# Performance work log

Measured on AMD Instinct MI355X. Metric: run time of the kernel, lower is better.

## Reference

```python
import jax, jax.numpy as jnp
import numpy as np

jax.config.update("jax_enable_x64", True)

# ---- physical constants (verbatim from source) ----
R = 0.000865
CONST = 2 * np.pi * R ** 3
C_SOUND = 343.0
RHO = 1.225
C1 = CONST * (1 / (6 * RHO * C_SOUND ** 2))
C2 = CONST * (-RHO / 4)
AREA = 0.0008
F = 40000.0
KWAV = 2 * np.pi / (C_SOUND / F)
W = 2 * np.pi * F
U = 3.086
M = 64
N = 64
B = 32768


def _h_of_r(rnorm):
    # h(r) = Area * (j rho c k) * u * exp(-j k r) / (2 pi r)
    return AREA * (1j * RHO * C_SOUND * KWAV) * U * np.exp(-1j * KWAV * rnorm) / (2 * np.pi * rnorm)


def _build_operators():
    # 8x8 transducer array (1cm pitch) at z=0; 8x8 focal points at z=0.10m
    xs = (np.arange(8) - 3.5) * 0.01
    gx, gy = np.meshgrid(xs, xs, indexing="ij")
    sensor_positions = np.stack([gx.ravel(), gy.ravel(), np.zeros(N)], axis=1)  # [n,3]
    fx = (np.arange(8) - 3.5) * 0.005
    px, py = np.meshgrid(fx, fx, indexing="ij")
    point_positions = np.stack([px.ravel(), py.ravel(), np.full(M, 0.10)], axis=1)  # [m,3]

    diff = point_positions[:, None, :] - sensor_positions[None, :, :]  # [m,n,3]
    r = np.linalg.norm(diff, axis=-1)
    h = _h_of_r(r)  # [m,n] complex128 (row vector h_matrices[i][0,:])

    delta = 1e-6
    q = np.empty((M, 3, N), dtype=np.complex128)
    for d in range(3):
        e = np.zeros(3)
        e[d] = delta
        rp = np.linalg.norm(diff + e, axis=-1)
        rm = np.linalg.norm(diff - e, axis=-1)
        q[:, d, :] = (-1 / (1j * W * RHO)) * (_h_of_r(rp) - _h_of_r(rm)) / (2 * delta)
    return h, q


def setup_inputs() -> dict:
    key = jax.random.key(0)
    k1, k2, k3 = jax.random.split(key, 3)
    pred_amplitude = jax.random.uniform(k1, (B, N), dtype=jnp.float32)
    pred_phase = jax.random.uniform(k2, (B, N), dtype=jnp.float32) * (2 * np.pi)
    true_energy = jax.random.normal(k3, (B, M), dtype=jnp.float32)
    h_np, q_np = _build_operators()
    return {
        "pred_amplitude": pred_amplitude,
        "pred_phase": pred_phase,
        "true_energy": true_energy,
        "h": jnp.asarray(h_np),  # [m,n] complex128
        "q": jnp.asarray(q_np),  # [m,3,n] complex128
    }


def reference(pred_amplitude, pred_phase, true_energy, h, q):
    # A_b = amplitude * exp(j*phase), cast to complex128 as in the source
    A = (pred_amplitude * jnp.exp(1j * pred_phase.astype(jnp.complex64))).astype(jnp.complex128)  # [B,n]
    # E[b,i] = Re( A^H (c1 h_i^H h_i + c2 q_i^H q_i) A )
    #        = c1 |h_i . A_b|^2 + c2 ||q_i A_b||^2   (rank-1 / rank-3 quadratic forms)
    hA = jnp.einsum("mn,bn->bm", h, A)          # [B,m]
    qA = jnp.einsum("mdn,bn->bmd", q, A)        # [B,m,3]
    E = C1 * (jnp.abs(hA) ** 2) + C2 * jnp.sum(jnp.abs(qA) ** 2, axis=-1)  # [B,m] real
    pred_energy = (E * 100000.0).astype(jnp.float32)
    return jnp.mean((pred_energy - true_energy) ** 2)
```

## Files before the change

kernel.cpp:

```cpp
#include <hip/hip_runtime.h>
#include <hip/hip_bf16.h>


typedef short s16x8 __attribute__((ext_vector_type(8)));
typedef float f32x4 __attribute__((ext_vector_type(4)));
typedef unsigned int u32x4 __attribute__((ext_vector_type(4)));

#define B_TOTAL 32768

constexpr double PI_ = 3.14159265358979323846;
constexpr double RHO_ = 1.225, CS_ = 343.0, FREQ_ = 40000.0, UU_ = 3.086, AREA_ = 0.0008;
constexpr double KW_ = 2.0 * PI_ * FREQ_ / CS_;
constexpr double WW_ = 2.0 * PI_ * FREQ_;
constexpr double RR_ = 0.000865;
constexpr double CONSTV_ = 2.0 * PI_ * RR_ * RR_ * RR_;
constexpr double C1E5_ = CONSTV_ / (6.0 * RHO_ * CS_ * CS_) * 100000.0;
constexpr double C2E5_ = CONSTV_ * RHO_ / 4.0 * 100000.0;
constexpr double GG_ = AREA_ * RHO_ * CS_ * KW_ * UU_ / (2.0 * PI_);

__device__ inline unsigned int pk2(float a, float b) {
    __hip_bfloat162 h = __float22bfloat162_rn(make_float2(a, b));
    unsigned int u;
    __builtin_memcpy(&u, &h, 4);
    return u;
}

__device__ inline void poly_sincos(float u, float& s, float& c) {
    float u2 = u * u;
    float sp = fmaf(u2, -7.6471637e-13f, 1.6059044e-10f);
    sp = fmaf(u2, sp, -2.5052108e-8f);
    sp = fmaf(u2, sp, 2.7557319e-6f);
    sp = fmaf(u2, sp, -1.9841270e-4f);
    sp = fmaf(u2, sp, 8.3333335e-3f);
    sp = fmaf(u2, sp, -0.16666667f);
    s = u * fmaf(u2, sp, 1.0f);
    float cp = fmaf(u2, -1.1470746e-11f, 2.0876757e-9f);
    cp = fmaf(u2, cp, -2.7557319e-7f);
    cp = fmaf(u2, cp, 2.4801587e-5f);
    cp = fmaf(u2, cp, -1.3888889e-3f);
    cp = fmaf(u2, cp, 4.1666668e-2f);
    cp = fmaf(u2, cp, -0.5f);
    c = fmaf(u2, cp, 1.0f);
}

__device__ inline void sincos_2pit(float t, float& s, float& c) {
    float x = t - rintf(t);
    poly_sincos(x * 6.2831853e+0f, s, c);
}

__device__ inline void sincos_rad(float p, float& s, float& c) {
    const float INV2PI = 0.15915494309189535f;
    float n = rintf(p * INV2PI);
    poly_sincos(fmaf(n, -6.2831853e+0f, p), s, c);
}

__global__ __launch_bounds__(512, 2)
void fused_energy(const float* __restrict__ amp, const float* __restrict__ ph,
                  const float* __restrict__ te,
                  double* __restrict__ partials) {
    __shared__ unsigned short Wl[512 * 128];
    __shared__ unsigned short Xt[2][32 * 128];
    __shared__ double sred[8];

    const int t = threadIdx.x;
    const int wave = t >> 6, lane = t & 63;
    const int lrow = lane & 15, lkgrp = lane >> 4;
    const int wr = wave & 3, wc = wave >> 2;
    const int blk = blockIdx.x;
    const int xc = t >> 4, xn4 = t & 15;

    const int baseA = (blk * 128 + xc) * 64 + xn4 * 4;
    float4 am0 = *reinterpret_cast<const float4*>(amp + baseA);
    float4 pv0 = *reinterpret_cast<const float4*>(ph + baseA);
    float4 amCur = *reinterpret_cast<const float4*>(amp + baseA + 32 * 64);
    float4 pvCur = *reinterpret_cast<const float4*>(ph + baseA + 32 * 64);
    const int teB = (blk * 128 + wc * 16 + lrow) * 64 + wr * 16 + (lkgrp >> 1);
    float teU[8], teN[8];
#pragma unroll
    for (int rt = 0; rt < 8; ++rt) teU[rt] = te[teB + rt * 2];

    {
        const float G1 = sqrtf((float)C1E5_) * (float)GG_;
        const float G2 = sqrtf((float)C2E5_) * (float)(GG_ / (WW_ * RHO_));
        const float KWf = (float)KW_;
        const float REVf = (float)(FREQ_ / CS_);
        int mm = t >> 3, nx = t & 7;
        int mx = mm >> 3, my = mm & 7;
        float dx = ((float)mx - 3.5f) * 0.005f - ((float)nx - 3.5f) * 0.01f;
        const float dz = 0.10f;
        u32x4 pkp[16];
#pragma unroll
        for (int j2 = 0; j2 < 4; ++j2) {
            float va[8], vb[8];
#pragma unroll
            for (int jj = 0; jj < 2; ++jj) {
                int j = j2 * 2 + jj;
                float dy = ((float)my - 3.5f) * 0.005f - ((float)j - 3.5f) * 0.01f;
                float r2 = dx * dx + dy * dy + dz * dz;
                float r = sqrtf(r2);
                float invr = 1.0f / r;
                float kr = KWf * r;
                float S, C;
                sincos_2pit(REVf * r, S, C);
                float hb = G1 * invr;
                float qb = G2 * invr * invr * invr;
                float t1 = kr * S + C, t2 = kr * C - S;
                float* v = jj ? vb : va;
                v[0] = hb * S;      v[1] = hb * C;
                v[2] = qb * dx * t1; v[3] = qb * dx * t2;
                v[4] = qb * dy * t1; v[5] = qb * dy * t2;
                v[6] = qb * dz * t1; v[7] = qb * dz * t2;
            }
            const int  rs[16] = {0,1,1,0, 2,3,3,2, 4,5,5,4, 6,7,7,6};
            const bool rn[16] = {false,true,false,false, false,true,false,false,
                                 false,true,false,false, false,true,false,false};
#pragma unroll
            for (int r = 0; r < 16; ++r) {
                float a = va[rs[r]], b = vb[rs[r]];
                pkp[r][j2] = rn[r] ? pk2(-a, -b) : pk2(a, b);
            }
        }
#pragma unroll
        for (int r8 = 0; r8 < 8; ++r8) {
            int row = mm * 8 + r8;
            int swz = (((row >> 3) ^ row) & 7) << 4;
            char* base = reinterpret_cast<char*>(Wl) + row * 256;
            *reinterpret_cast<u32x4*>(base + ((nx * 16) ^ swz)) = pkp[r8 * 2];
            *reinterpret_cast<u32x4*>(base + ((nx * 16 + 128) ^ swz)) = pkp[r8 * 2 + 1];
        }
    }

    auto buildX = [&](int bb, const float4& a4, const float4& p4) {
        float s0, c0, s1, c1, s2, c2, s3, c3;
        sincos_rad(p4.x, s0, c0);
        sincos_rad(p4.y, s1, c1);
        sincos_rad(p4.z, s2, c2);
        sincos_rad(p4.w, s3, c3);
        unsigned int re01 = pk2(a4.x * c0, a4.y * c1);
        unsigned int re23 = pk2(a4.z * c2, a4.w * c3);
        unsigned int im01 = pk2(a4.x * s0, a4.y * s1);
        unsigned int im23 = pk2(a4.z * s2, a4.w * s3);
        int swz = (xc & 7) << 4;
        char* rowp = reinterpret_cast<char*>(Xt[bb]) + xc * 256;
        *reinterpret_cast<uint2*>(rowp + ((xn4 * 8) ^ swz)) = make_uint2(re01, re23);
        *reinterpret_cast<uint2*>(rowp + ((128 + xn4 * 8) ^ swz)) = make_uint2(im01, im23);
    };

    buildX(0, am0, pv0);
    __syncthreads();

    s16x8 wf[8][4];
#pragma unroll
    for (int rt = 0; rt < 8; ++rt) {
        int row = wr * 128 + rt * 16 + lrow;
        int swz = (((row >> 3) ^ row) & 7) << 4;
        const char* base = reinterpret_cast<const char*>(Wl) + row * 256;
#pragma unroll
        for (int kk = 0; kk < 4; ++kk)
            wf[rt][kk] = *reinterpret_cast<const s16x8*>(base + ((kk * 64 + lkgrp * 16) ^ swz));
    }

    float lpart = 0.f;

#pragma unroll
    for (int it = 0; it < 4; ++it) {
        s16x8 xf[4];
        {
            int c = wc * 16 + lrow;
            int swz = (c & 7) << 4;
            const char* rowp = reinterpret_cast<const char*>(Xt[it & 1]) + c * 256;
#pragma unroll
            for (int kk = 0; kk < 4; ++kk)
                xf[kk] = *reinterpret_cast<const s16x8*>(rowp + ((kk * 64 + lkgrp * 16) ^ swz));
        }
        float4 amN, pvN;
        if (it < 2) {
            int off = baseA + (it + 2) * 32 * 64;
            amN = *reinterpret_cast<const float4*>(amp + off);
            pvN = *reinterpret_cast<const float4*>(ph + off);
        }
        if (it < 3) {
            int off = teB + (it + 1) * 32 * 64;
#pragma unroll
            for (int rt = 0; rt < 8; ++rt) teN[rt] = te[off + rt * 2];
        }
        f32x4 acc[8];
#pragma unroll
        for (int rt = 0; rt < 8; ++rt) {
            acc[rt] = {0.f, 0.f, 0.f, 0.f};
#pragma unroll
            for (int kk = 0; kk < 4; ++kk)
                acc[rt] = __builtin_amdgcn_mfma_f32_16x16x32_bf16(wf[rt][kk], xf[kk],
                                                                  acc[rt], 0, 0, 0);
        }
        if (it < 3) buildX((it + 1) & 1, amCur, pvCur);
#pragma unroll
        for (int rt = 0; rt < 8; ++rt) {
            float q0 = acc[rt].x * acc[rt].x;
            float q1 = acc[rt].y * acc[rt].y;
            float q2 = acc[rt].z * acc[rt].z;
            float q3 = acc[rt].w * acc[rt].w;
            float part = (lkgrp & 1) ? (-(q0 + q1 + q2 + q3)) : (q0 + q1 - q2 - q3);
            float pred = part + __shfl_xor(part, 16);
            float d = pred - teU[rt];
            lpart = fmaf(0.5f * d, d, lpart);
        }
        if (it < 2) { amCur = amN; pvCur = pvN; }
        if (it < 3) {
#pragma unroll
            for (int rt = 0; rt < 8; ++rt) teU[rt] = teN[rt];
            __syncthreads();
        }
    }

#pragma unroll
    for (int off = 32; off >= 1; off >>= 1)
        lpart += __shfl_xor(lpart, off);
    if (lane == 0) sred[wave] = (double)lpart;
    __syncthreads();
    if (t == 0)
        partials[blk] = sred[0] + sred[1] + sred[2] + sred[3] +
                        sred[4] + sred[5] + sred[6] + sred[7];
}

__global__ void finalize(const double* __restrict__ partials,
                         float* __restrict__ out) {
    __shared__ double sred[4];
    const int t = threadIdx.x;
    const int wave = t >> 6, lane = t & 63;
    double v = partials[t];
#pragma unroll
    for (int off = 32; off >= 1; off >>= 1)
        v += __shfl_xor(v, off);
    if (lane == 0) sred[wave] = v;
    __syncthreads();
    if (t == 0)
        out[0] = (float)((sred[0] + sred[1] + sred[2] + sred[3]) /
                         (double)(B_TOTAL * 64));
}

extern "C" void kernel_launch(void* const* d_in, const int* in_sizes, int n_in,
                              void* d_out, int out_size, void* d_ws, size_t ws_size,
                              hipStream_t stream) {
    const float* amp = (const float*)d_in[0];
    const float* ph  = (const float*)d_in[1];
    const float* te  = (const float*)d_in[2];

    double* partials = (double*)d_ws;

    fused_energy<<<256, 512, 0, stream>>>(amp, ph, te, partials);
    finalize<<<1, 256, 0, stream>>>(partials, (float*)d_out);
}
```

Before: 18.31 us.

## Halve the LDS weight matrix by exploiting the complex structure and double the grid

Only half of the real-expanded complex weight matrix is stored in LDS (Re and -Im parts). Each lane rebuilds the other half of its MFMA operands at load time by swapping the K halves and flipping the bf16 sign bits. The block shrinks to 256 threads over 64 batch rows, and the grid grows to 512 blocks so the fixed per-block weight-building cost is spread across more CUs. Each block now computes half as many weight entries, but the per-block setup still makes up a larger share of each block's work, and the finalize kernel has to reduce 512 partials.

```diff
diff --git a/kernel.cpp b/kernel.cpp
--- a/kernel.cpp
+++ b/kernel.cpp
@@ -23,6 +23,15 @@
     unsigned int u;
     __builtin_memcpy(&u, &h, 4);
     return u;
+}
+
+__device__ inline s16x8 negbf(s16x8 x) {
+    u32x4 u;
+    __builtin_memcpy(&u, &x, 16);
+    u ^= (u32x4){0x80008000u, 0x80008000u, 0x80008000u, 0x80008000u};
+    s16x8 r;
+    __builtin_memcpy(&r, &u, 16);
+    return r;
 }
 
 __device__ inline void poly_sincos(float u, float& s, float& c) {
@@ -54,27 +63,26 @@
     poly_sincos(fmaf(n, -6.2831853e+0f, p), s, c);
 }
 
-__global__ __launch_bounds__(512, 2)
+__global__ __launch_bounds__(256, 2)
 void fused_energy(const float* __restrict__ amp, const float* __restrict__ ph,
                   const float* __restrict__ te,
                   double* __restrict__ partials) {
-    __shared__ unsigned short Wl[512 * 128];
-    __shared__ unsigned short Xt[2][32 * 128];
-    __shared__ double sred[8];
+    __shared__ unsigned short Wl[256 * 128];
+    __shared__ unsigned short Xt[2][16 * 128];
+    __shared__ double sred[4];
 
     const int t = threadIdx.x;
     const int wave = t >> 6, lane = t & 63;
     const int lrow = lane & 15, lkgrp = lane >> 4;
-    const int wr = wave & 3, wc = wave >> 2;
     const int blk = blockIdx.x;
     const int xc = t >> 4, xn4 = t & 15;
 
-    const int baseA = (blk * 128 + xc) * 64 + xn4 * 4;
+    const int baseA = (blk * 64 + xc) * 64 + xn4 * 4;
     float4 am0 = *reinterpret_cast<const float4*>(amp + baseA);
     float4 pv0 = *reinterpret_cast<const float4*>(ph + baseA);
-    float4 amCur = *reinterpret_cast<const float4*>(amp + baseA + 32 * 64);
-    float4 pvCur = *reinterpret_cast<const float4*>(ph + baseA + 32 * 64);
-    const int teB = (blk * 128 + wc * 16 + lrow) * 64 + wr * 16 + (lkgrp >> 1);
+    float4 amCur = *reinterpret_cast<const float4*>(amp + baseA + 16 * 64);
+    float4 pvCur = *reinterpret_cast<const float4*>(ph + baseA + 16 * 64);
+    const int teB = (blk * 64 + lrow) * 64 + wave * 16 + (lkgrp >> 1);
     float teU[8], teN[8];
 #pragma unroll
     for (int rt = 0; rt < 8; ++rt) teU[rt] = te[teB + rt * 2];
@@ -84,18 +92,19 @@
         const float G2 = sqrtf((float)C2E5_) * (float)(GG_ / (WW_ * RHO_));
         const float KWf = (float)KW_;
         const float REVf = (float)(FREQ_ / CS_);
-        int mm = t >> 3, nx = t & 7;
+        int mm = t >> 2, nq = t & 3;
         int mx = mm >> 3, my = mm & 7;
-        float dx = ((float)mx - 3.5f) * 0.005f - ((float)nx - 3.5f) * 0.01f;
         const float dz = 0.10f;
-        u32x4 pkp[16];
-#pragma unroll
-        for (int j2 = 0; j2 < 4; ++j2) {
+        u32x4 pkp[4][2][2];
+#pragma unroll
+        for (int jp = 0; jp < 8; ++jp) {
             float va[8], vb[8];
 #pragma unroll
             for (int jj = 0; jj < 2; ++jj) {
-                int j = j2 * 2 + jj;
-                float dy = ((float)my - 3.5f) * 0.005f - ((float)j - 3.5f) * 0.01f;
+                int j = jp * 2 + jj;
+                int sx = nq * 2 + (j >> 3), sy = j & 7;
+                float dx = ((float)mx - 3.5f) * 0.005f - ((float)sx - 3.5f) * 0.01f;
+                float dy = ((float)my - 3.5f) * 0.005f - ((float)sy - 3.5f) * 0.01f;
                 float r2 = dx * dx + dy * dy + dz * dz;
                 float r = sqrtf(r2);
                 float invr = 1.0f / r;
@@ -106,27 +115,28 @@
                 float qb = G2 * invr * invr * invr;
                 float t1 = kr * S + C, t2 = kr * C - S;
                 float* v = jj ? vb : va;
-                v[0] = hb * S;      v[1] = hb * C;
+                v[0] = hb * S;       v[1] = hb * C;
                 v[2] = qb * dx * t1; v[3] = qb * dx * t2;
                 v[4] = qb * dy * t1; v[5] = qb * dy * t2;
                 v[6] = qb * dz * t1; v[7] = qb * dz * t2;
             }
-            const int  rs[16] = {0,1,1,0, 2,3,3,2, 4,5,5,4, 6,7,7,6};
-            const bool rn[16] = {false,true,false,false, false,true,false,false,
-                                 false,true,false,false, false,true,false,false};
-#pragma unroll
-            for (int r = 0; r < 16; ++r) {
-                float a = va[rs[r]], b = vb[rs[r]];
-                pkp[r][j2] = rn[r] ? pk2(-a, -b) : pk2(a, b);
+#pragma unroll
+            for (int c2 = 0; c2 < 4; ++c2) {
+                pkp[c2][0][jp >> 2][jp & 3] = pk2(va[2 * c2], vb[2 * c2]);
+                pkp[c2][1][jp >> 2][jp & 3] = pk2(-va[2 * c2 + 1], -vb[2 * c2 + 1]);
             }
         }
 #pragma unroll
-        for (int r8 = 0; r8 < 8; ++r8) {
-            int row = mm * 8 + r8;
-            int swz = (((row >> 3) ^ row) & 7) << 4;
-            char* base = reinterpret_cast<char*>(Wl) + row * 256;
-            *reinterpret_cast<u32x4*>(base + ((nx * 16) ^ swz)) = pkp[r8 * 2];
-            *reinterpret_cast<u32x4*>(base + ((nx * 16 + 128) ^ swz)) = pkp[r8 * 2 + 1];
+        for (int c2 = 0; c2 < 4; ++c2) {
+            int srow = mm * 4 + c2;
+            int swz = (((srow >> 3) ^ srow) & 7) << 4;
+            char* base = reinterpret_cast<char*>(Wl) + srow * 256;
+#pragma unroll
+            for (int h = 0; h < 2; ++h)
+#pragma unroll
+                for (int jg = 0; jg < 2; ++jg)
+                    *reinterpret_cast<u32x4*>(
+                        base + ((h * 128 + nq * 32 + jg * 16) ^ swz)) = pkp[c2][h][jg];
         }
     }
 
@@ -152,12 +162,20 @@
     s16x8 wf[8][4];
 #pragma unroll
     for (int rt = 0; rt < 8; ++rt) {
-        int row = wr * 128 + rt * 16 + lrow;
-        int swz = (((row >> 3) ^ row) & 7) << 4;
-        const char* base = reinterpret_cast<const char*>(Wl) + row * 256;
+        int row = wave * 128 + rt * 16 + lrow;
+        int srow = (row >> 3) * 4 + ((lrow & 7) >> 1);
+        int p = lrow & 1;
+        int swz = (((srow >> 3) ^ srow) & 7) << 4;
+        const char* base = reinterpret_cast<const char*>(Wl) + srow * 256;
+        s16x8 st[4];
 #pragma unroll
         for (int kk = 0; kk < 4; ++kk)
-            wf[rt][kk] = *reinterpret_cast<const s16x8*>(base + ((kk * 64 + lkgrp * 16) ^ swz));
+            st[kk] = *reinterpret_cast<const s16x8*>(
+                base + ((kk * 64 + lkgrp * 16) ^ swz));
+        wf[rt][0] = p ? negbf(st[2]) : st[0];
+        wf[rt][1] = p ? negbf(st[3]) : st[1];
+        wf[rt][2] = p ? st[0] : st[2];
+        wf[rt][3] = p ? st[1] : st[3];
     }
 
     float lpart = 0.f;
@@ -166,21 +184,21 @@
     for (int it = 0; it < 4; ++it) {
         s16x8 xf[4];
         {
-            int c = wc * 16 + lrow;
-            int swz = (c & 7) << 4;
-            const char* rowp = reinterpret_cast<const char*>(Xt[it & 1]) + c * 256;
+            int swz = (lrow & 7) << 4;
+            const char* rowp = reinterpret_cast<const char*>(Xt[it & 1]) + lrow * 256;
 #pragma unroll
             for (int kk = 0; kk < 4; ++kk)
-                xf[kk] = *reinterpret_cast<const s16x8*>(rowp + ((kk * 64 + lkgrp * 16) ^ swz));
+                xf[kk] = *reinterpret_cast<const s16x8*>(
+                    rowp + ((kk * 64 + lkgrp * 16) ^ swz));
         }
         float4 amN, pvN;
         if (it < 2) {
-            int off = baseA + (it + 2) * 32 * 64;
+            int off = baseA + (it + 2) * 16 * 64;
             amN = *reinterpret_cast<const float4*>(amp + off);
             pvN = *reinterpret_cast<const float4*>(ph + off);
         }
         if (it < 3) {
-            int off = teB + (it + 1) * 32 * 64;
+            int off = teB + (it + 1) * 16 * 64;
 #pragma unroll
             for (int rt = 0; rt < 8; ++rt) teN[rt] = te[off + rt * 2];
         }
@@ -219,13 +237,12 @@
     if (lane == 0) sred[wave] = (double)lpart;
     __syncthreads();
     if (t == 0)
-        partials[blk] = sred[0] + sred[1] + sred[2] + sred[3] +
-                        sred[4] + sred[5] + sred[6] + sred[7];
+        partials[blk] = sred[0] + sred[1] + sred[2] + sred[3];
 }
 
 __global__ void finalize(const double* __restrict__ partials,
                          float* __restrict__ out) {
-    __shared__ double sred[4];
+    __shared__ double sred[8];
     const int t = threadIdx.x;
     const int wave = t >> 6, lane = t & 63;
     double v = partials[t];
@@ -235,7 +252,8 @@
     if (lane == 0) sred[wave] = v;
     __syncthreads();
     if (t == 0)
-        out[0] = (float)((sred[0] + sred[1] + sred[2] + sred[3]) /
+        out[0] = (float)((sred[0] + sred[1] + sred[2] + sred[3] +
+                          sred[4] + sred[5] + sred[6] + sred[7]) /
                          (double)(B_TOTAL * 64));
 }
 
@@ -248,6 +266,6 @@
 
     double* partials = (double*)d_ws;
 
-    fused_energy<<<256, 512, 0, stream>>>(amp, ph, te, partials);
-    finalize<<<1, 256, 0, stream>>>(partials, (float*)d_out);
-}
+    fused_energy<<<512, 256, 0, stream>>>(amp, ph, te, partials);
+    finalize<<<1, 512, 0, stream>>>(partials, (float*)d_out);
+}
```

Measured after the change: 19.55 us. 6.8% more time.
